# Kernel tuning notes

Measured on AMD Instinct MI355X. Metric: run time of the kernel, lower is better.

Reference implementation:

```python
import jax, jax.numpy as jnp
import numpy as np

ALPHA = 1.702
LIMIT = 7.0
H = 2880      # hidden_size
D = 2880      # expert_dim (intermediate_size)
E = 8         # num_local_experts
B, S = 1, 1024


def setup_inputs() -> dict:
    key = jax.random.key(0)
    k1, k2, k3, k4, k5, k6 = jax.random.split(key, 6)
    scale = 1.0 / np.sqrt(H)
    return {
        "hidden_states": jax.random.normal(k1, (B, S, H), dtype=jnp.float32),
        "routing_weights": jax.random.uniform(k2, (B * S, E), dtype=jnp.float32),
        "gate_up_proj": jax.random.normal(k3, (E, H, 2 * D), dtype=jnp.float32) * scale,
        "gate_up_proj_bias": jax.random.normal(k4, (E, 2 * D), dtype=jnp.float32) * 0.02,
        "down_proj": jax.random.normal(k5, (E, D, H), dtype=jnp.float32) * (1.0 / np.sqrt(D)),
        "down_proj_bias": jax.random.normal(k6, (E, H), dtype=jnp.float32) * 0.02,
    }


def reference(hidden_states, routing_weights, gate_up_proj, gate_up_proj_bias,
              down_proj, down_proj_bias):
    b, s, h = hidden_states.shape
    x = hidden_states.reshape(-1, h)                       # [T, H]
    # Dense all-experts formulation (faithful to original): every expert sees every token.
    gate_up = jnp.einsum('th,ehd->etd', x, gate_up_proj) + gate_up_proj_bias[:, None, :]  # [E,T,2D]
    gate = gate_up[..., ::2]                               # interleaved split
    up = gate_up[..., 1::2]
    gate = jnp.minimum(gate, LIMIT)
    up = jnp.clip(up, -LIMIT, LIMIT)
    glu = gate * jax.nn.sigmoid(gate * ALPHA)
    out = jnp.einsum('etd,edh->eth', (up + 1.0) * glu, down_proj) + down_proj_bias[:, None, :]  # [E,T,H]
    # combine with routing weights: routing_weights [T,E] -> [E,T,1]
    out = out * routing_weights.T[:, :, None]
    y = out.sum(axis=0)                                    # [T, H]
    return y.reshape(b, s, h)
```

## Files before the change

kernel.cpp:

```cpp
#include <hip/hip_runtime.h>

namespace {

constexpr int T     = 1024;
constexpr int HDIM  = 2880;
constexpr int DDIM  = 2880;
constexpr int NE    = 8;
constexpr int TWO_D = 5760;
constexpr float ALPHA = 1.702f;
constexpr float LIMIT = 7.0f;

constexpr int LDSS = 40;

typedef __attribute__((ext_vector_type(8))) short bf16x8;
typedef __attribute__((ext_vector_type(4))) unsigned short u16x4;
typedef __attribute__((ext_vector_type(4))) float f32x4;

__device__ __forceinline__ unsigned short f2bf(float f) {
  union { float f; unsigned u; } x; x.f = f;
  unsigned u = x.u;
  u += 0x7fffu + ((u >> 16) & 1u);
  return (unsigned short)(u >> 16);
}

}

__global__ void init_bias_kernel(const float* __restrict__ RW,
                                 const float* __restrict__ B2,
                                 float* __restrict__ Y) {
  int h = blockIdx.x * 64 + threadIdx.x;
  int t = blockIdx.y;
  float s = 0.f;
#pragma unroll
  for (int e = 0; e < NE; ++e) s += RW[t * NE + e] * B2[e * HDIM + h];
  Y[(size_t)t * HDIM + h] = s;
}

__global__ __launch_bounds__(256) void gemm1_act_kernel(
    const float* __restrict__ X,
    const float* __restrict__ W1,
    const float* __restrict__ B1,
    const float* __restrict__ RW,
    unsigned short* __restrict__ A)
{
  __shared__ __align__(16) unsigned short lA[128 * LDSS];
  __shared__ __align__(16) unsigned short lB[128 * LDSS];

  const int tid = threadIdx.x;
  const int m0 = blockIdx.x * 128;
  const int n0 = blockIdx.y * 128;
  const int e  = blockIdx.z;
  const float* Wp = W1 + (size_t)e * HDIM * TWO_D;

  f32x4 acc[4][4];
#pragma unroll
  for (int i = 0; i < 4; ++i)
#pragma unroll
    for (int j = 0; j < 4; ++j) acc[i][j] = (f32x4)0.f;

  const int w    = tid >> 6;
  const int lane = tid & 63;
  const int wm   = w & 1, wn = w >> 1;
  const int r    = lane & 15, q = lane >> 4;

  const int sa_m = tid >> 3;
  const int sa_q = tid & 7;
  const int sb_n = tid & 127;
  const int sb_k = tid >> 7;

  for (int kt = 0; kt < HDIM / 32; ++kt) {
    const int k0g = kt * 32;

#pragma unroll
    for (int it = 0; it < 4; ++it) {
      int m = sa_m + it * 32;
      const f32x4 v = *(const f32x4*)(X + (size_t)(m0 + m) * HDIM + k0g + sa_q * 4);
      u16x4 pv = { f2bf(v.x), f2bf(v.y), f2bf(v.z), f2bf(v.w) };
      *(u16x4*)(&lA[m * LDSS + sa_q * 4]) = pv;
    }

#pragma unroll
    for (int it = 0; it < 2; ++it) {
      int k0 = (sb_k + it * 2) * 8;
      float f[8];
#pragma unroll
      for (int rr = 0; rr < 8; ++rr)
        f[rr] = Wp[(size_t)(k0g + k0 + rr) * TWO_D + n0 + sb_n];
      bf16x8 pv = { (short)f2bf(f[0]), (short)f2bf(f[1]), (short)f2bf(f[2]), (short)f2bf(f[3]),
                    (short)f2bf(f[4]), (short)f2bf(f[5]), (short)f2bf(f[6]), (short)f2bf(f[7]) };
      *(bf16x8*)(&lB[sb_n * LDSS + k0]) = pv;
    }

    __syncthreads();

    const unsigned short* pA = &lA[(wm * 64 + r) * LDSS + q * 8];
    const unsigned short* pB = &lB[(wn * 64 + r) * LDSS + q * 8];
    bf16x8 af[4], bfr[4];
#pragma unroll
    for (int i = 0; i < 4; ++i) af[i]  = *(const bf16x8*)(pA + i * 16 * LDSS);
#pragma unroll
    for (int j = 0; j < 4; ++j) bfr[j] = *(const bf16x8*)(pB + j * 16 * LDSS);
#pragma unroll
    for (int i = 0; i < 4; ++i)
#pragma unroll
      for (int j = 0; j < 4; ++j)
        acc[i][j] = __builtin_amdgcn_mfma_f32_16x16x32_bf16(af[i], bfr[j], acc[i][j], 0, 0, 0);

    __syncthreads();
  }

  const float* bp = B1 + (size_t)e * TWO_D;
#pragma unroll
  for (int i = 0; i < 4; ++i) {
    const int mb = m0 + wm * 64 + i * 16 + q * 4;
    float rwv[4];
#pragma unroll
    for (int p = 0; p < 4; ++p) rwv[p] = RW[(mb + p) * NE + e];
#pragma unroll
    for (int j = 0; j < 4; ++j) {
      const int c = n0 + wn * 64 + j * 16 + r;
      const float bias = bp[c];
#pragma unroll
      for (int p = 0; p < 4; ++p) {
        float v = acc[i][j][p] + bias;
        float o = __shfl_xor(v, 1, 64);
        float gate = (r & 1) ? o : v;
        float up   = (r & 1) ? v : o;
        gate = fminf(gate, LIMIT);
        up   = fminf(fmaxf(up, -LIMIT), LIMIT);
        float glu = gate / (1.f + __expf(-ALPHA * gate));
        float a   = (up + 1.f) * glu * rwv[p];
        if ((r & 1) == 0) {
          int d = c >> 1;
          A[(size_t)e * T * DDIM + (size_t)(mb + p) * DDIM + d] = f2bf(a);
        }
      }
    }
  }
}

__global__ __launch_bounds__(256) void gemm2_acc_kernel(
    const unsigned short* __restrict__ A,
    const float* __restrict__ W2,
    float* __restrict__ Y)
{
  __shared__ __align__(16) unsigned short lA[128 * LDSS];
  __shared__ __align__(16) unsigned short lB[128 * LDSS];

  const int tid = threadIdx.x;
  const int m0 = blockIdx.x * 128;
  const int n0 = blockIdx.y * 128;
  const int e  = blockIdx.z;
  const float* Wp = W2 + (size_t)e * DDIM * HDIM;
  const unsigned short* Ap = A + (size_t)e * T * DDIM;

  f32x4 acc[4][4];
#pragma unroll
  for (int i = 0; i < 4; ++i)
#pragma unroll
    for (int j = 0; j < 4; ++j) acc[i][j] = (f32x4)0.f;

  const int w    = tid >> 6;
  const int lane = tid & 63;
  const int wm   = w & 1, wn = w >> 1;
  const int r    = lane & 15, q = lane >> 4;

  const int sa_m = tid >> 2;
  const int sa_c = tid & 3;
  const int sb_n = tid & 127;
  const int sb_k = tid >> 7;

  for (int kt = 0; kt < DDIM / 32; ++kt) {
    const int k0g = kt * 32;

#pragma unroll
    for (int it = 0; it < 2; ++it) {
      int m = sa_m + it * 64;
      bf16x8 v = *(const bf16x8*)(Ap + (size_t)(m0 + m) * DDIM + k0g + sa_c * 8);
      *(bf16x8*)(&lA[m * LDSS + sa_c * 8]) = v;
    }

    int col = n0 + sb_n;
    if (col > HDIM - 1) col = HDIM - 1;
#pragma unroll
    for (int it = 0; it < 2; ++it) {
      int k0 = (sb_k + it * 2) * 8;
      float f[8];
#pragma unroll
      for (int rr = 0; rr < 8; ++rr)
        f[rr] = Wp[(size_t)(k0g + k0 + rr) * HDIM + col];
      bf16x8 pv = { (short)f2bf(f[0]), (short)f2bf(f[1]), (short)f2bf(f[2]), (short)f2bf(f[3]),
                    (short)f2bf(f[4]), (short)f2bf(f[5]), (short)f2bf(f[6]), (short)f2bf(f[7]) };
      *(bf16x8*)(&lB[sb_n * LDSS + k0]) = pv;
    }

    __syncthreads();

    const unsigned short* pA = &lA[(wm * 64 + r) * LDSS + q * 8];
    const unsigned short* pB = &lB[(wn * 64 + r) * LDSS + q * 8];
    bf16x8 af[4], bfr[4];
#pragma unroll
    for (int i = 0; i < 4; ++i) af[i]  = *(const bf16x8*)(pA + i * 16 * LDSS);
#pragma unroll
    for (int j = 0; j < 4; ++j) bfr[j] = *(const bf16x8*)(pB + j * 16 * LDSS);
#pragma unroll
    for (int i = 0; i < 4; ++i)
#pragma unroll
      for (int j = 0; j < 4; ++j)
        acc[i][j] = __builtin_amdgcn_mfma_f32_16x16x32_bf16(af[i], bfr[j], acc[i][j], 0, 0, 0);

    __syncthreads();
  }

#pragma unroll
  for (int i = 0; i < 4; ++i) {
    const int mb = m0 + wm * 64 + i * 16 + q * 4;
#pragma unroll
    for (int j = 0; j < 4; ++j) {
      const int h = n0 + wn * 64 + j * 16 + r;
      if (h < HDIM) {
#pragma unroll
        for (int p = 0; p < 4; ++p)
          atomicAdd(&Y[(size_t)(mb + p) * HDIM + h], acc[i][j][p]);
      }
    }
  }
}

extern "C" void kernel_launch(void* const* d_in, const int* in_sizes, int n_in,
                              void* d_out, int out_size, void* d_ws, size_t ws_size,
                              hipStream_t stream) {
  const float* X  = (const float*)d_in[0];
  const float* RW = (const float*)d_in[1];
  const float* W1 = (const float*)d_in[2];
  const float* B1 = (const float*)d_in[3];
  const float* W2 = (const float*)d_in[4];
  const float* B2 = (const float*)d_in[5];
  float* Y = (float*)d_out;
  unsigned short* Abuf = (unsigned short*)d_ws;

  hipLaunchKernelGGL(init_bias_kernel, dim3(45, 1024), dim3(64), 0, stream, RW, B2, Y);
  hipLaunchKernelGGL(gemm1_act_kernel, dim3(8, 45, 8), dim3(256), 0, stream, X, W1, B1, RW, Abuf);
  hipLaunchKernelGGL(gemm2_acc_kernel, dim3(8, 23, 8), dim3(256), 0, stream, Abuf, W2, Y);
}
```

Before: 1.690 ms.

## Pre-transpose weights to bf16 and stream GEMM tiles directly into LDS

Adds pre-passes that convert X to bf16 and transpose-and-convert both expert weight tensors into K-contiguous bf16 layouts on every call. Both GEMMs then fill their shared-memory tiles with direct global-to-LDS 16-byte loads instead of strided fp32 loads and in-register conversion. The second GEMM writes per-expert partial outputs to a buffer rather than using atomics, and a final kernel sums the experts and adds the routed bias. In exchange it moves over a gigabyte of extra weight traffic per call and needs a workspace of roughly half a gigabyte. If the workspace is smaller, it falls back to the old path.

New measurement: 1.556 ms. 1.09x faster.

```diff
diff --git a/kernel.cpp b/kernel.cpp
--- a/kernel.cpp
+++ b/kernel.cpp
@@ -23,34 +23,79 @@
   return (unsigned short)(u >> 16);
 }
 
-}
-
-__global__ void init_bias_kernel(const float* __restrict__ RW,
-                                 const float* __restrict__ B2,
-                                 float* __restrict__ Y) {
-  int h = blockIdx.x * 64 + threadIdx.x;
-  int t = blockIdx.y;
-  float s = 0.f;
-#pragma unroll
-  for (int e = 0; e < NE; ++e) s += RW[t * NE + e] * B2[e * HDIM + h];
-  Y[(size_t)t * HDIM + h] = s;
-}
-
-__global__ __launch_bounds__(256) void gemm1_act_kernel(
-    const float* __restrict__ X,
-    const float* __restrict__ W1,
+__device__ __forceinline__ void async16(const void* g, void* l) {
+  __builtin_amdgcn_global_load_lds(
+      (const __attribute__((address_space(1))) unsigned int*)g,
+      (__attribute__((address_space(3))) unsigned int*)l, 16, 0, 0);
+}
+
+}
+
+
+__global__ __launch_bounds__(256) void cvt_x_kernel(const float* __restrict__ X,
+                                                    unsigned short* __restrict__ Xb) {
+  const int i = (blockIdx.x * 256 + threadIdx.x) * 8;
+  const f32x4 a = *(const f32x4*)(X + i);
+  const f32x4 b = *(const f32x4*)(X + i + 4);
+  bf16x8 pv;
+  pv[0] = (short)f2bf(a.x); pv[1] = (short)f2bf(a.y);
+  pv[2] = (short)f2bf(a.z); pv[3] = (short)f2bf(a.w);
+  pv[4] = (short)f2bf(b.x); pv[5] = (short)f2bf(b.y);
+  pv[6] = (short)f2bf(b.z); pv[7] = (short)f2bf(b.w);
+  *(bf16x8*)(Xb + i) = pv;
+}
+
+__global__ __launch_bounds__(256) void transpose_cvt_kernel(
+    const float* __restrict__ src, unsigned short* __restrict__ dst,
+    int R, int C) {
+  __shared__ __align__(16) unsigned short lt[64][70];
+  const size_t eo = (size_t)blockIdx.z * R * C;
+  const float* sp = src + eo;
+  unsigned short* dp = dst + eo;
+  const int c0 = blockIdx.x * 64;
+  const int r0 = blockIdx.y * 64;
+  const int t  = threadIdx.x;
+
+  const int lr = t >> 4;
+  const int lc = (t & 15) * 4;
+#pragma unroll
+  for (int it = 0; it < 4; ++it) {
+    const int rr = lr + it * 16;
+    const f32x4 v = *(const f32x4*)(sp + (size_t)(r0 + rr) * C + c0 + lc);
+    const unsigned w0 = (unsigned)f2bf(v.x) | ((unsigned)f2bf(v.y) << 16);
+    const unsigned w1 = (unsigned)f2bf(v.z) | ((unsigned)f2bf(v.w) << 16);
+    *(unsigned*)(&lt[rr][lc])     = w0;
+    *(unsigned*)(&lt[rr][lc + 2]) = w1;
+  }
+  __syncthreads();
+
+  const int dr  = (t & 7) * 8;
+  const int dcb = t >> 3;
+#pragma unroll
+  for (int it = 0; it < 2; ++it) {
+    const int c = dcb + it * 32;
+    bf16x8 ov;
+#pragma unroll
+    for (int j = 0; j < 8; ++j) ov[j] = (short)lt[dr + j][c];
+    *(bf16x8*)(dp + (size_t)(c0 + c) * R + r0 + dr) = ov;
+  }
+}
+
+__global__ __launch_bounds__(256) void gemm1_fast(
+    const unsigned short* __restrict__ Xb,
+    const unsigned short* __restrict__ W1T,
     const float* __restrict__ B1,
     const float* __restrict__ RW,
     unsigned short* __restrict__ A)
 {
-  __shared__ __align__(16) unsigned short lA[128 * LDSS];
-  __shared__ __align__(16) unsigned short lB[128 * LDSS];
+  __shared__ __align__(16) unsigned short lA[128 * 32];
+  __shared__ __align__(16) unsigned short lB[128 * 32];
 
   const int tid = threadIdx.x;
   const int m0 = blockIdx.x * 128;
   const int n0 = blockIdx.y * 128;
   const int e  = blockIdx.z;
-  const float* Wp = W1 + (size_t)e * HDIM * TWO_D;
+  const unsigned short* Wp = W1T + (size_t)e * TWO_D * HDIM;
 
   f32x4 acc[4][4];
 #pragma unroll
@@ -63,43 +108,28 @@
   const int wm   = w & 1, wn = w >> 1;
   const int r    = lane & 15, q = lane >> 4;
 
-  const int sa_m = tid >> 3;
-  const int sa_q = tid & 7;
-  const int sb_n = tid & 127;
-  const int sb_k = tid >> 7;
+  const int srow = lane >> 2;
+  const int skc  = (lane & 3) * 8;
+  const unsigned short* ga = Xb + (size_t)(m0 + w * 32 + srow) * HDIM + skc;
+  const unsigned short* gb = Wp + (size_t)(n0 + w * 32 + srow) * HDIM + skc;
+  unsigned short* la0 = lA + (w * 2) * 512;
+  unsigned short* lb0 = lB + (w * 2) * 512;
 
   for (int kt = 0; kt < HDIM / 32; ++kt) {
-    const int k0g = kt * 32;
-
-#pragma unroll
-    for (int it = 0; it < 4; ++it) {
-      int m = sa_m + it * 32;
-      const f32x4 v = *(const f32x4*)(X + (size_t)(m0 + m) * HDIM + k0g + sa_q * 4);
-      u16x4 pv = { f2bf(v.x), f2bf(v.y), f2bf(v.z), f2bf(v.w) };
-      *(u16x4*)(&lA[m * LDSS + sa_q * 4]) = pv;
-    }
-
-#pragma unroll
-    for (int it = 0; it < 2; ++it) {
-      int k0 = (sb_k + it * 2) * 8;
-      float f[8];
-#pragma unroll
-      for (int rr = 0; rr < 8; ++rr)
-        f[rr] = Wp[(size_t)(k0g + k0 + rr) * TWO_D + n0 + sb_n];
-      bf16x8 pv = { (short)f2bf(f[0]), (short)f2bf(f[1]), (short)f2bf(f[2]), (short)f2bf(f[3]),
-                    (short)f2bf(f[4]), (short)f2bf(f[5]), (short)f2bf(f[6]), (short)f2bf(f[7]) };
-      *(bf16x8*)(&lB[sb_n * LDSS + k0]) = pv;
-    }
-
-    __syncthreads();
-
-    const unsigned short* pA = &lA[(wm * 64 + r) * LDSS + q * 8];
-    const unsigned short* pB = &lB[(wn * 64 + r) * LDSS + q * 8];
+    const int k0 = kt * 32;
+    async16(ga + k0,                        la0);
+    async16(ga + (size_t)16 * HDIM + k0,    la0 + 512);
+    async16(gb + k0,                        lb0);
+    async16(gb + (size_t)16 * HDIM + k0,    lb0 + 512);
+    __syncthreads();
+
+    const unsigned short* pA = &lA[(wm * 64 + r) * 32 + q * 8];
+    const unsigned short* pB = &lB[(wn * 64 + r) * 32 + q * 8];
     bf16x8 af[4], bfr[4];
 #pragma unroll
-    for (int i = 0; i < 4; ++i) af[i]  = *(const bf16x8*)(pA + i * 16 * LDSS);
-#pragma unroll
-    for (int j = 0; j < 4; ++j) bfr[j] = *(const bf16x8*)(pB + j * 16 * LDSS);
+    for (int i = 0; i < 4; ++i) af[i]  = *(const bf16x8*)(pA + i * 512);
+#pragma unroll
+    for (int j = 0; j < 4; ++j) bfr[j] = *(const bf16x8*)(pB + j * 512);
 #pragma unroll
     for (int i = 0; i < 4; ++i)
 #pragma unroll
@@ -139,47 +169,230 @@
   }
 }
 
-__global__ __launch_bounds__(256) void gemm2_acc_kernel(
+__global__ __launch_bounds__(256) void gemm2_fast(
     const unsigned short* __restrict__ A,
-    const float* __restrict__ W2,
-    float* __restrict__ Y)
+    const unsigned short* __restrict__ W2T,
+    float* __restrict__ Yp)
 {
+  __shared__ __align__(16) unsigned short lA[128 * 32];
+  __shared__ __align__(16) unsigned short lB[128 * 32];
+
+  const int tid = threadIdx.x;
+  const int m0 = blockIdx.x * 128;
+  const int n0 = blockIdx.y * 128;
+  const int e  = blockIdx.z;
+  const unsigned short* Ap = A   + (size_t)e * T * DDIM;
+  const unsigned short* Wp = W2T + (size_t)e * HDIM * DDIM;
+
+  f32x4 acc[4][4];
+#pragma unroll
+  for (int i = 0; i < 4; ++i)
+#pragma unroll
+    for (int j = 0; j < 4; ++j) acc[i][j] = (f32x4)0.f;
+
+  const int w    = tid >> 6;
+  const int lane = tid & 63;
+  const int wm   = w & 1, wn = w >> 1;
+  const int r    = lane & 15, q = lane >> 4;
+
+  const int srow = lane >> 2;
+  const int skc  = (lane & 3) * 8;
+  int br0 = n0 + w * 32 + srow;
+  int br1 = br0 + 16;
+  if (br0 > HDIM - 1) br0 = HDIM - 1;
+  if (br1 > HDIM - 1) br1 = HDIM - 1;
+  const unsigned short* ga  = Ap + (size_t)(m0 + w * 32 + srow) * DDIM + skc;
+  const unsigned short* gb0 = Wp + (size_t)br0 * DDIM + skc;
+  const unsigned short* gb1 = Wp + (size_t)br1 * DDIM + skc;
+  unsigned short* la0 = lA + (w * 2) * 512;
+  unsigned short* lb0 = lB + (w * 2) * 512;
+
+  for (int kt = 0; kt < DDIM / 32; ++kt) {
+    const int k0 = kt * 32;
+    async16(ga  + k0,                     la0);
+    async16(ga  + (size_t)16 * DDIM + k0, la0 + 512);
+    async16(gb0 + k0,                     lb0);
+    async16(gb1 + k0,                     lb0 + 512);
+    __syncthreads();
+
+    const unsigned short* pA = &lA[(wm * 64 + r) * 32 + q * 8];
+    const unsigned short* pB = &lB[(wn * 64 + r) * 32 + q * 8];
+    bf16x8 af[4], bfr[4];
+#pragma unroll
+    for (int i = 0; i < 4; ++i) af[i]  = *(const bf16x8*)(pA + i * 512);
+#pragma unroll
+    for (int j = 0; j < 4; ++j) bfr[j] = *(const bf16x8*)(pB + j * 512);
+#pragma unroll
+    for (int i = 0; i < 4; ++i)
+#pragma unroll
+      for (int j = 0; j < 4; ++j)
+        acc[i][j] = __builtin_amdgcn_mfma_f32_16x16x32_bf16(af[i], bfr[j], acc[i][j], 0, 0, 0);
+
+    __syncthreads();
+  }
+
+#pragma unroll
+  for (int i = 0; i < 4; ++i) {
+    const int mb = m0 + wm * 64 + i * 16 + q * 4;
+#pragma unroll
+    for (int j = 0; j < 4; ++j) {
+      const int h = n0 + wn * 64 + j * 16 + r;
+      if (h < HDIM) {
+#pragma unroll
+        for (int p = 0; p < 4; ++p)
+          Yp[((size_t)e * T + (mb + p)) * HDIM + h] = acc[i][j][p];
+      }
+    }
+  }
+}
+
+__global__ __launch_bounds__(256) void reduce_bias_kernel(
+    const float* __restrict__ Yp, const float* __restrict__ RW,
+    const float* __restrict__ B2, float* __restrict__ Y) {
+  const int idx = (blockIdx.x * 256 + threadIdx.x) * 4;
+  const int t = idx / HDIM;
+  const int h = idx - t * HDIM;
+  f32x4 s = (f32x4)0.f;
+#pragma unroll
+  for (int e = 0; e < NE; ++e) {
+    const f32x4 v = *(const f32x4*)(Yp + ((size_t)e * T + t) * HDIM + h);
+    const f32x4 b = *(const f32x4*)(B2 + (size_t)e * HDIM + h);
+    const float rw = RW[t * NE + e];
+    s.x += v.x + rw * b.x;
+    s.y += v.y + rw * b.y;
+    s.z += v.z + rw * b.z;
+    s.w += v.w + rw * b.w;
+  }
+  *(f32x4*)(Y + idx) = s;
+}
+
+
+__global__ void init_bias_kernel(const float* __restrict__ RW,
+                                 const float* __restrict__ B2,
+                                 float* __restrict__ Y) {
+  int h = blockIdx.x * 64 + threadIdx.x;
+  int t = blockIdx.y;
+  float s = 0.f;
+#pragma unroll
+  for (int e = 0; e < NE; ++e) s += RW[t * NE + e] * B2[e * HDIM + h];
+  Y[(size_t)t * HDIM + h] = s;
+}
+
+__global__ __launch_bounds__(256) void gemm1_act_kernel(
+    const float* __restrict__ X, const float* __restrict__ W1,
+    const float* __restrict__ B1, const float* __restrict__ RW,
+    unsigned short* __restrict__ A) {
   __shared__ __align__(16) unsigned short lA[128 * LDSS];
   __shared__ __align__(16) unsigned short lB[128 * LDSS];
-
+  const int tid = threadIdx.x;
+  const int m0 = blockIdx.x * 128;
+  const int n0 = blockIdx.y * 128;
+  const int e  = blockIdx.z;
+  const float* Wp = W1 + (size_t)e * HDIM * TWO_D;
+  f32x4 acc[4][4];
+#pragma unroll
+  for (int i = 0; i < 4; ++i)
+#pragma unroll
+    for (int j = 0; j < 4; ++j) acc[i][j] = (f32x4)0.f;
+  const int w = tid >> 6, lane = tid & 63;
+  const int wm = w & 1, wn = w >> 1;
+  const int r = lane & 15, q = lane >> 4;
+  const int sa_m = tid >> 3, sa_q = tid & 7;
+  const int sb_n = tid & 127, sb_k = tid >> 7;
+  for (int kt = 0; kt < HDIM / 32; ++kt) {
+    const int k0g = kt * 32;
+#pragma unroll
+    for (int it = 0; it < 4; ++it) {
+      int m = sa_m + it * 32;
+      const f32x4 v = *(const f32x4*)(X + (size_t)(m0 + m) * HDIM + k0g + sa_q * 4);
+      u16x4 pv = { f2bf(v.x), f2bf(v.y), f2bf(v.z), f2bf(v.w) };
+      *(u16x4*)(&lA[m * LDSS + sa_q * 4]) = pv;
+    }
+#pragma unroll
+    for (int it = 0; it < 2; ++it) {
+      int k0 = (sb_k + it * 2) * 8;
+      float f[8];
+#pragma unroll
+      for (int rr = 0; rr < 8; ++rr)
+        f[rr] = Wp[(size_t)(k0g + k0 + rr) * TWO_D + n0 + sb_n];
+      bf16x8 pv = { (short)f2bf(f[0]), (short)f2bf(f[1]), (short)f2bf(f[2]), (short)f2bf(f[3]),
+                    (short)f2bf(f[4]), (short)f2bf(f[5]), (short)f2bf(f[6]), (short)f2bf(f[7]) };
+      *(bf16x8*)(&lB[sb_n * LDSS + k0]) = pv;
+    }
+    __syncthreads();
+    const unsigned short* pA = &lA[(wm * 64 + r) * LDSS + q * 8];
+    const unsigned short* pB = &lB[(wn * 64 + r) * LDSS + q * 8];
+    bf16x8 af[4], bfr[4];
+#pragma unroll
+    for (int i = 0; i < 4; ++i) af[i]  = *(const bf16x8*)(pA + i * 16 * LDSS);
+#pragma unroll
+    for (int j = 0; j < 4; ++j) bfr[j] = *(const bf16x8*)(pB + j * 16 * LDSS);
+#pragma unroll
+    for (int i = 0; i < 4; ++i)
+#pragma unroll
+      for (int j = 0; j < 4; ++j)
+        acc[i][j] = __builtin_amdgcn_mfma_f32_16x16x32_bf16(af[i], bfr[j], acc[i][j], 0, 0, 0);
+    __syncthreads();
+  }
+  const float* bp = B1 + (size_t)e * TWO_D;
+#pragma unroll
+  for (int i = 0; i < 4; ++i) {
+    const int mb = m0 + wm * 64 + i * 16 + q * 4;
+    float rwv[4];
+#pragma unroll
+    for (int p = 0; p < 4; ++p) rwv[p] = RW[(mb + p) * NE + e];
+#pragma unroll
+    for (int j = 0; j < 4; ++j) {
+      const int c = n0 + wn * 64 + j * 16 + r;
+      const float bias = bp[c];
+#pragma unroll
+      for (int p = 0; p < 4; ++p) {
+        float v = acc[i][j][p] + bias;
+        float o = __shfl_xor(v, 1, 64);
+        float gate = (r & 1) ? o : v;
+        float up   = (r & 1) ? v : o;
+        gate = fminf(gate, LIMIT);
+        up   = fminf(fmaxf(up, -LIMIT), LIMIT);
+        float glu = gate / (1.f + __expf(-ALPHA * gate));
+        float a   = (up + 1.f) * glu * rwv[p];
+        if ((r & 1) == 0) {
+          int d = c >> 1;
+          A[(size_t)e * T * DDIM + (size_t)(mb + p) * DDIM + d] = f2bf(a);
+        }
+      }
+    }
+  }
+}
+
+__global__ __launch_bounds__(256) void gemm2_acc_kernel(
+    const unsigned short* __restrict__ A, const float* __restrict__ W2,
+    float* __restrict__ Y) {
+  __shared__ __align__(16) unsigned short lA[128 * LDSS];
+  __shared__ __align__(16) unsigned short lB[128 * LDSS];
   const int tid = threadIdx.x;
   const int m0 = blockIdx.x * 128;
   const int n0 = blockIdx.y * 128;
   const int e  = blockIdx.z;
   const float* Wp = W2 + (size_t)e * DDIM * HDIM;
   const unsigned short* Ap = A + (size_t)e * T * DDIM;
-
   f32x4 acc[4][4];
 #pragma unroll
   for (int i = 0; i < 4; ++i)
 #pragma unroll
     for (int j = 0; j < 4; ++j) acc[i][j] = (f32x4)0.f;
-
-  const int w    = tid >> 6;
-  const int lane = tid & 63;
-  const int wm   = w & 1, wn = w >> 1;
-  const int r    = lane & 15, q = lane >> 4;
-
-  const int sa_m = tid >> 2;
-  const int sa_c = tid & 3;
-  const int sb_n = tid & 127;
-  const int sb_k = tid >> 7;
-
+  const int w = tid >> 6, lane = tid & 63;
+  const int wm = w & 1, wn = w >> 1;
+  const int r = lane & 15, q = lane >> 4;
+  const int sa_m = tid >> 2, sa_c = tid & 3;
+  const int sb_n = tid & 127, sb_k = tid >> 7;
   for (int kt = 0; kt < DDIM / 32; ++kt) {
     const int k0g = kt * 32;
-
 #pragma unroll
     for (int it = 0; it < 2; ++it) {
       int m = sa_m + it * 64;
       bf16x8 v = *(const bf16x8*)(Ap + (size_t)(m0 + m) * DDIM + k0g + sa_c * 8);
       *(bf16x8*)(&lA[m * LDSS + sa_c * 8]) = v;
     }
-
     int col = n0 + sb_n;
     if (col > HDIM - 1) col = HDIM - 1;
 #pragma unroll
@@ -193,9 +406,7 @@
                     (short)f2bf(f[4]), (short)f2bf(f[5]), (short)f2bf(f[6]), (short)f2bf(f[7]) };
       *(bf16x8*)(&lB[sb_n * LDSS + k0]) = pv;
     }
-
-    __syncthreads();
-
+    __syncthreads();
     const unsigned short* pA = &lA[(wm * 64 + r) * LDSS + q * 8];
     const unsigned short* pB = &lB[(wn * 64 + r) * LDSS + q * 8];
     bf16x8 af[4], bfr[4];
@@ -208,10 +419,8 @@
 #pragma unroll
       for (int j = 0; j < 4; ++j)
         acc[i][j] = __builtin_amdgcn_mfma_f32_16x16x32_bf16(af[i], bfr[j], acc[i][j], 0, 0, 0);
-
-    __syncthreads();
-  }
-
+    __syncthreads();
+  }
 #pragma unroll
   for (int i = 0; i < 4; ++i) {
     const int mb = m0 + wm * 64 + i * 16 + q * 4;
@@ -237,9 +446,37 @@
   const float* W2 = (const float*)d_in[4];
   const float* B2 = (const float*)d_in[5];
   float* Y = (float*)d_out;
-  unsigned short* Abuf = (unsigned short*)d_ws;
-
-  hipLaunchKernelGGL(init_bias_kernel, dim3(45, 1024), dim3(64), 0, stream, RW, B2, Y);
-  hipLaunchKernelGGL(gemm1_act_kernel, dim3(8, 45, 8), dim3(256), 0, stream, X, W1, B1, RW, Abuf);
-  hipLaunchKernelGGL(gemm2_acc_kernel, dim3(8, 23, 8), dim3(256), 0, stream, Abuf, W2, Y);
-}
+
+  constexpr size_t XB_B  = (size_t)T * HDIM * 2;
+  constexpr size_t AB_B  = (size_t)NE * T * DDIM * 2;
+  constexpr size_t W1T_B = (size_t)NE * TWO_D * HDIM * 2;
+  constexpr size_t W2T_B = (size_t)NE * HDIM * DDIM * 2;
+  constexpr size_t YP_B  = (size_t)NE * T * HDIM * 4;
+  constexpr size_t NEED  = XB_B + AB_B + W1T_B + W2T_B + YP_B;
+
+  if (ws_size >= NEED) {
+    char* p = (char*)d_ws;
+    unsigned short* Xb  = (unsigned short*)p; p += XB_B;
+    unsigned short* Ab  = (unsigned short*)p; p += AB_B;
+    unsigned short* W1T = (unsigned short*)p; p += W1T_B;
+    unsigned short* W2T = (unsigned short*)p; p += W2T_B;
+    float* Yp = (float*)p;
+
+    hipLaunchKernelGGL(cvt_x_kernel, dim3((T * HDIM) / 2048), dim3(256), 0, stream, X, Xb);
+    hipLaunchKernelGGL(transpose_cvt_kernel, dim3(TWO_D / 64, HDIM / 64, NE), dim3(256), 0, stream,
+                       W1, W1T, HDIM, TWO_D);
+    hipLaunchKernelGGL(transpose_cvt_kernel, dim3(HDIM / 64, DDIM / 64, NE), dim3(256), 0, stream,
+                       W2, W2T, DDIM, HDIM);
+    hipLaunchKernelGGL(gemm1_fast, dim3(T / 128, TWO_D / 128, NE), dim3(256), 0, stream,
+                       Xb, W1T, B1, RW, Ab);
+    hipLaunchKernelGGL(gemm2_fast, dim3(T / 128, (HDIM + 127) / 128, NE), dim3(256), 0, stream,
+                       Ab, W2T, Yp);
+    hipLaunchKernelGGL(reduce_bias_kernel, dim3((T * HDIM) / 1024), dim3(256), 0, stream,
+                       Yp, RW, B2, Y);
+  } else {
+    unsigned short* Abuf = (unsigned short*)d_ws;
+    hipLaunchKernelGGL(init_bias_kernel, dim3(45, 1024), dim3(64), 0, stream, RW, B2, Y);
+    hipLaunchKernelGGL(gemm1_act_kernel, dim3(8, 45, 8), dim3(256), 0, stream, X, W1, B1, RW, Abuf);
+    hipLaunchKernelGGL(gemm2_acc_kernel, dim3(8, 23, 8), dim3(256), 0, stream, Abuf, W2, Y);
+  }
+}
```
